# Optimization experiments

Hardware: AMD Instinct MI355X
Metric: run time of the kernel (lower is better)

Reference implementation:

```python
import jax, jax.numpy as jnp
import numpy as np

# Chambolle-Pock / Condat over-relaxed primal-dual constants (from _TVDenoiser.__init__)
TAU = 0.01
RHO = 1.99
SIGMA = 1.0 / TAU / 8.0  # 1/tau/8, 8 = Lipschitz const of D^T D in 2D
THS = 0.1                # lambda (denoise threshold)
NITER = 40
CRIT = 1e-5


def nabla2(x):
    """Forward finite differences: x (..., H, W) -> u (..., H, W, 2).
    Channel 0: diff along H (rows), channel 1: diff along W (cols); last
    row/col of each channel is zero (as in the deepinv original)."""
    dh = jnp.zeros_like(x).at[..., :-1, :].set(x[..., 1:, :] - x[..., :-1, :])
    dw = jnp.zeros_like(x).at[..., :, :-1].set(x[..., :, 1:] - x[..., :, :-1])
    return jnp.stack([dh, dw], axis=-1)


def nabla2_adjoint(u):
    """Adjoint of nabla2: u (..., H, W, 2) -> (..., H, W)."""
    v0 = u[..., :-1, :, 0]  # (..., H-1, W)
    v1 = u[..., :, :-1, 1]  # (..., H, W-1)
    out = jnp.zeros(u.shape[:-1], u.dtype)
    out = out.at[..., :-1, :].add(-v0).at[..., 1:, :].add(v0)
    out = out.at[..., :, :-1].add(-v1).at[..., :, 1:].add(v1)
    return out


def _step(x2, u2, y):
    # prox_tau_fx: (x + tau*y)/(1+tau)
    x = (x2 - TAU * nabla2_adjoint(u2) + TAU * y) / (1.0 + TAU)
    # prox_sigma_g_conj: project gradient field onto L2 ball of radius lambda
    v = u2 + SIGMA * nabla2(2.0 * x - x2)
    mag = jnp.sqrt(jnp.sum(v * v, axis=-1))  # (..., H, W)
    u = v / jnp.maximum(mag / THS, 1.0)[..., None]
    # over-relaxation
    x2n = x2 + RHO * (x - x2)
    u2n = u2 + RHO * (u - u2)
    return x2n, u2n


def setup_inputs() -> dict:
    key = jax.random.key(0)
    y = jax.random.normal(key, (8, 512, 512), dtype=jnp.float32)
    return {"y": y}


def reference(y):
    # warm restart init: x2 = y, u2 = 0 (restart branch of forward)
    u0 = jnp.zeros(y.shape + (2,), y.dtype)

    def cond(state):
        x2, u2, it, rel = state
        # original breaks at end of iteration _ if _ > 1 and rel_err < crit
        return (it < NITER) & jnp.logical_not((it >= 3) & (rel < CRIT))

    def body(state):
        x2, u2, it, _ = state
        x2n, u2n = _step(x2, u2, y)
        rel = jnp.linalg.norm((x2 - x2n).ravel()) / jnp.linalg.norm(
            x2n.ravel() + 1e-12
        )
        return (x2n, u2n, it + 1, rel)

    x2, u2, it, rel = jax.lax.while_loop(
        cond, body, (y, u0, jnp.int32(0), jnp.float32(jnp.inf))
    )
    return x2
```

## Files before the change

kernel.cpp:

```cpp
#include <hip/hip_runtime.h>


#define Hh 512
#define Ww 512
#define Bb 8
#define TS 48
#define KF 8
#define S  64
#define NT 512
#define RS 8

__global__ __launch_bounds__(NT, 3)
void tv_packed(const float*  __restrict__ y_in,
               const float4* __restrict__ st_in,
               float4* __restrict__ st_out,
               float*  __restrict__ x2_out,
               int first, int last)
{
    constexpr float TAU = 0.01f;
    constexpr float RHO = 1.99f;
    constexpr float HRHO = 0.995f;
    constexpr float SIGMA = 12.5f;
    constexpr float THS = 0.1f;
    constexpr float INV_1PT = 1.0f / 1.01f;

    __shared__ float u0B [9 * S];
    __shared__ float wTop[9 * S];

    const int b   = blockIdx.z;
    const int r0  = blockIdx.y * TS;
    const int c0  = blockIdx.x * TS;
    const int tid = threadIdx.x;
    const size_t plane = (size_t)b * (Hh * Ww);

    const int s   = tid >> 6;
    const int lc  = tid & 63;
    const int gc  = c0 - KF + lc;
    const bool colin = (gc >= 0) & (gc < Ww);
    const float sewf = (gc < Ww - 1) ? SIGMA : 0.f;
    const int lr0 = RS * s;
    const int gr0 = r0 - KF + lr0;
    const float sigBot = (gr0 + RS - 1 == Hh - 1) ? 0.f : SIGMA;

    if (tid < S) { u0B[tid] = 0.f; wTop[8 * S + tid] = 0.f; }

    float u0[RS], u1[RS], x2[RS], yv[RS], w[RS];
    unsigned tmp0 = 0u, tmp1 = 0u;

    #pragma unroll
    for (int i = 0; i < RS; ++i) {
        const int gr = gr0 + i;
        const int lr = lr0 + i;
        const bool img = colin & (gr >= 0) & (gr < Hh);
        const size_t gi = img ? (plane + (size_t)gr * Ww + gc) : plane;
        if (first) {
            float c = y_in[gi];
            c = img ? c : 0.f;
            x2[i] = c; yv[i] = c; u0[i] = 0.f; u1[i] = 0.f;
        } else {
            float4 st = st_in[gi];
            x2[i] = img ? st.x : 0.f;
            u0[i] = img ? st.y : 0.f;
            u1[i] = img ? st.z : 0.f;
            yv[i] = img ? st.w : 0.f;
        }
        unsigned tm = img ? (unsigned)min(min(lr, S - 1 - lr), min(lc, S - 1 - lc)) : 0u;
        if (i < 4) tmp0 |= tm << (8 * i);
        else       tmp1 |= tm << (8 * (i - 4));
    }
    u0B[(s + 1) * S + lc] = u0[RS - 1];
    __syncthreads();

    for (int t = 0; t < KF; ++t) {
        {
            float u0a = u0B[s * S + lc];
            #pragma unroll
            for (int i = 0; i < RS; ++i) {
                float ul = __shfl_up(u1[i], 1, 64);
                float ua = (i == 0) ? u0a : u0[i - 1];
                float adj = ua - u0[i] + ul - u1[i];
                float xv = fmaf(TAU, yv[i] - adj, x2[i]);
                w[i] = fmaf(2.0f * INV_1PT, xv, -x2[i]);
            }
            wTop[s * S + lc] = w[0];
        }
        __syncthreads();
        {
            float wbot = wTop[(s + 1) * S + lc];
            #pragma unroll
            for (int i = 0; i < RS; ++i) {
                float wr = __shfl_down(w[i], 1, 64);
                float wb = (i == RS - 1) ? wbot : w[i + 1];
                const float sig_h = (i == RS - 1) ? sigBot : SIGMA;
                float v0 = fmaf(sig_h, wb - w[i], u0[i]);
                float v1 = fmaf(sewf,  wr - w[i], u1[i]);
                float iv = fminf(THS * __builtin_amdgcn_rsqf(fmaf(v0, v0, v1 * v1)), 1.f);
                unsigned tmb = ((i < 4 ? tmp0 : tmp1) >> (8 * (i & 3))) & 255u;
                bool act = (unsigned)t < tmb;
                float r1 = act ? RHO  : 0.f;
                float rh = act ? HRHO : 0.f;
                u0[i] = fmaf(r1, fmaf(v0, iv, -u0[i]), u0[i]);
                u1[i] = fmaf(r1, fmaf(v1, iv, -u1[i]), u1[i]);
                x2[i] = fmaf(rh, w[i] - x2[i], x2[i]);
            }
            u0B[(s + 1) * S + lc] = u0[RS - 1];
        }
        __syncthreads();
    }

    if (s >= 1 && s <= 6 && lc >= KF && lc < KF + TS && gc < Ww) {
        #pragma unroll
        for (int i = 0; i < RS; ++i) {
            const int gr = gr0 + i;
            if (gr < Hh) {
                const size_t gi = plane + (size_t)gr * Ww + gc;
                if (last) x2_out[gi] = x2[i];
                else      st_out[gi] = make_float4(x2[i], u0[i], u1[i], yv[i]);
            }
        }
    }
}

__global__ __launch_bounds__(NT, 3)
void tv_sep(const float*  __restrict__ x2_in,
            const float2* __restrict__ u_in,
            const float*  __restrict__ y_in,
            float*  __restrict__ x2_out,
            float2* __restrict__ u_out,
            int first, int last)
{
    constexpr float TAU = 0.01f;
    constexpr float RHO = 1.99f;
    constexpr float HRHO = 0.995f;
    constexpr float SIGMA = 12.5f;
    constexpr float THS = 0.1f;
    constexpr float INV_1PT = 1.0f / 1.01f;

    __shared__ float u0B [9 * S];
    __shared__ float wTop[9 * S];

    const int b   = blockIdx.z;
    const int r0  = blockIdx.y * TS;
    const int c0  = blockIdx.x * TS;
    const int tid = threadIdx.x;
    const size_t plane = (size_t)b * (Hh * Ww);

    const int s   = tid >> 6;
    const int lc  = tid & 63;
    const int gc  = c0 - KF + lc;
    const bool colin = (gc >= 0) & (gc < Ww);
    const float sewf = (gc < Ww - 1) ? SIGMA : 0.f;
    const int lr0 = RS * s;
    const int gr0 = r0 - KF + lr0;
    const float sigBot = (gr0 + RS - 1 == Hh - 1) ? 0.f : SIGMA;

    if (tid < S) { u0B[tid] = 0.f; wTop[8 * S + tid] = 0.f; }

    float u0[RS], u1[RS], x2[RS], yv[RS], w[RS];
    unsigned tmp0 = 0u, tmp1 = 0u;

    #pragma unroll
    for (int i = 0; i < RS; ++i) {
        const int gr = gr0 + i;
        const int lr = lr0 + i;
        const bool img = colin & (gr >= 0) & (gr < Hh);
        float a = 0.f, c = 0.f, z0 = 0.f, z1 = 0.f;
        if (img) {
            size_t gi = plane + (size_t)gr * Ww + gc;
            c = y_in[gi];
            if (first) a = c;
            else {
                a = x2_in[gi];
                float2 uu = u_in[gi];
                z0 = uu.x; z1 = uu.y;
            }
        }
        u0[i] = z0; u1[i] = z1; x2[i] = a; yv[i] = c;
        unsigned tm = img ? (unsigned)min(min(lr, S - 1 - lr), min(lc, S - 1 - lc)) : 0u;
        if (i < 4) tmp0 |= tm << (8 * i);
        else       tmp1 |= tm << (8 * (i - 4));
    }
    u0B[(s + 1) * S + lc] = u0[RS - 1];
    __syncthreads();

    for (int t = 0; t < KF; ++t) {
        {
            float u0a = u0B[s * S + lc];
            #pragma unroll
            for (int i = 0; i < RS; ++i) {
                float ul = __shfl_up(u1[i], 1, 64);
                float ua = (i == 0) ? u0a : u0[i - 1];
                float adj = ua - u0[i] + ul - u1[i];
                float xv = fmaf(TAU, yv[i] - adj, x2[i]);
                w[i] = fmaf(2.0f * INV_1PT, xv, -x2[i]);
            }
            wTop[s * S + lc] = w[0];
        }
        __syncthreads();
        {
            float wbot = wTop[(s + 1) * S + lc];
            #pragma unroll
            for (int i = 0; i < RS; ++i) {
                float wr = __shfl_down(w[i], 1, 64);
                float wb = (i == RS - 1) ? wbot : w[i + 1];
                const float sig_h = (i == RS - 1) ? sigBot : SIGMA;
                float v0 = fmaf(sig_h, wb - w[i], u0[i]);
                float v1 = fmaf(sewf,  wr - w[i], u1[i]);
                float iv = fminf(THS * __builtin_amdgcn_rsqf(fmaf(v0, v0, v1 * v1)), 1.f);
                unsigned tmb = ((i < 4 ? tmp0 : tmp1) >> (8 * (i & 3))) & 255u;
                bool act = (unsigned)t < tmb;
                float r1 = act ? RHO  : 0.f;
                float rh = act ? HRHO : 0.f;
                u0[i] = fmaf(r1, fmaf(v0, iv, -u0[i]), u0[i]);
                u1[i] = fmaf(r1, fmaf(v1, iv, -u1[i]), u1[i]);
                x2[i] = fmaf(rh, w[i] - x2[i], x2[i]);
            }
            u0B[(s + 1) * S + lc] = u0[RS - 1];
        }
        __syncthreads();
    }

    if (s >= 1 && s <= 6 && lc >= KF && lc < KF + TS && gc < Ww) {
        #pragma unroll
        for (int i = 0; i < RS; ++i) {
            const int gr = gr0 + i;
            if (gr < Hh) {
                size_t gi = plane + (size_t)gr * Ww + gc;
                x2_out[gi] = x2[i];
                if (!last) u_out[gi] = make_float2(u0[i], u1[i]);
            }
        }
    }
}

extern "C" void kernel_launch(void* const* d_in, const int* in_sizes, int n_in,
                              void* d_out, int out_size, void* d_ws, size_t ws_size,
                              hipStream_t stream)
{
    const float* y = (const float*)d_in[0];
    float* out = (float*)d_out;
    const size_t NP = (size_t)Bb * Hh * Ww;

    dim3 grid((Ww + TS - 1) / TS, (Hh + TS - 1) / TS, Bb);

    if (ws_size >= 2 * NP * sizeof(float4)) {
        float4* stA = (float4*)d_ws;
        float4* stB = stA + NP;
        tv_packed<<<grid, NT, 0, stream>>>(y, stB, stA, out, 1, 0);
        tv_packed<<<grid, NT, 0, stream>>>(y, stA, stB, out, 0, 0);
        tv_packed<<<grid, NT, 0, stream>>>(y, stB, stA, out, 0, 0);
        tv_packed<<<grid, NT, 0, stream>>>(y, stA, stB, out, 0, 0);
        tv_packed<<<grid, NT, 0, stream>>>(y, stB, stA, out, 0, 1);
    } else {
        float*  ws  = (float*)d_ws;
        float*  x2A = ws;
        float*  x2B = ws + NP;
        float2* uA  = (float2*)(ws + 2 * NP);
        float2* uB  = (float2*)(ws + 4 * NP);
        tv_sep<<<grid, NT, 0, stream>>>(y,   uB, y, x2A, uA, 1, 0);
        tv_sep<<<grid, NT, 0, stream>>>(x2A, uA, y, x2B, uB, 0, 0);
        tv_sep<<<grid, NT, 0, stream>>>(x2B, uB, y, x2A, uA, 0, 0);
        tv_sep<<<grid, NT, 0, stream>>>(x2A, uA, y, x2B, uB, 0, 0);
        tv_sep<<<grid, NT, 0, stream>>>(x2B, uB, y, out, uA, 0, 1);
    }
}
```

Before: 223.2 us.

## Widen packed-state tiles to two columns per thread to cut halo overhead

Each thread in the packed kernel now processes two adjacent columns, widening the block tile to 128 columns with a 112-column interior. This reduces the fraction of redundant halo computation in the temporally blocked stencil. The cost is double the per-thread registers, launch bounds lowered to two blocks per SM, and fewer blocks in the grid, with a partially filled last column tile.

```diff
diff --git a/kernel.cpp b/kernel.cpp
--- a/kernel.cpp
+++ b/kernel.cpp
@@ -4,13 +4,15 @@
 #define Hh 512
 #define Ww 512
 #define Bb 8
-#define TS 48
+#define TSC 112
+#define TSR 48
 #define KF 8
-#define S  64
+#define SC 128
+#define SR 64
 #define NT 512
 #define RS 8
 
-__global__ __launch_bounds__(NT, 3)
+__global__ __launch_bounds__(NT, 2)
 void tv_packed(const float*  __restrict__ y_in,
                const float4* __restrict__ st_in,
                float4* __restrict__ st_out,
@@ -24,6 +26,156 @@
     constexpr float THS = 0.1f;
     constexpr float INV_1PT = 1.0f / 1.01f;
 
+    __shared__ float u0B [9 * SC];
+    __shared__ float wTop[9 * SC];
+
+    const int b   = blockIdx.z;
+    const int r0  = blockIdx.y * TSR;
+    const int c0  = blockIdx.x * TSC;
+    const int tid = threadIdx.x;
+    const size_t plane = (size_t)b * (Hh * Ww);
+
+    const int s     = tid >> 6;
+    const int lc    = tid & 63;
+    const int lcol0 = 2 * lc;
+    const int gc0   = c0 - KF + lcol0;
+    const bool colin0 = (gc0 >= 0) & (gc0 < Ww);
+    const bool colin1 = (gc0 + 1 >= 0) & (gc0 + 1 < Ww);
+    const float sewf0 = (gc0     < Ww - 1) ? SIGMA : 0.f;
+    const float sewf1 = (gc0 + 1 < Ww - 1) ? SIGMA : 0.f;
+    const int lr0 = RS * s;
+    const int gr0 = r0 - KF + lr0;
+    const float sigBot = (gr0 + RS - 1 == Hh - 1) ? 0.f : SIGMA;
+
+    if (tid < SC) { u0B[tid] = 0.f; wTop[8 * SC + tid] = 0.f; }
+
+    float x2[RS][2], u0[RS][2], u1[RS][2], yv[RS][2], w[RS][2];
+    unsigned tmp[4] = {0u, 0u, 0u, 0u};
+
+    #pragma unroll
+    for (int i = 0; i < RS; ++i) {
+        const int gr = gr0 + i;
+        const int lr = lr0 + i;
+        const bool rin = (gr >= 0) & (gr < Hh);
+        #pragma unroll
+        for (int c = 0; c < 2; ++c) {
+            const bool img = rin & (c ? colin1 : colin0);
+            const size_t gi = img ? (plane + (size_t)gr * Ww + (gc0 + c)) : plane;
+            if (first) {
+                float cy = y_in[gi]; cy = img ? cy : 0.f;
+                x2[i][c] = cy; yv[i][c] = cy; u0[i][c] = 0.f; u1[i][c] = 0.f;
+            } else {
+                float4 st = st_in[gi];
+                x2[i][c] = img ? st.x : 0.f;
+                u0[i][c] = img ? st.y : 0.f;
+                u1[i][c] = img ? st.z : 0.f;
+                yv[i][c] = img ? st.w : 0.f;
+            }
+            const int lcol = lcol0 + c;
+            unsigned tm = img ? (unsigned)min(min(lr, SR - 1 - lr),
+                                              min(lcol, SC - 1 - lcol)) : 0u;
+            const int k = 2 * i + c;
+            tmp[k >> 2] |= tm << (8 * (k & 3));
+        }
+    }
+    *(float2*)&u0B[(s + 1) * SC + lcol0] = make_float2(u0[RS - 1][0], u0[RS - 1][1]);
+    __syncthreads();
+
+    for (int t = 0; t < KF; ++t) {
+        {
+            float2 ua2 = *(float2*)&u0B[s * SC + lcol0];
+            #pragma unroll
+            for (int i = 0; i < RS; ++i) {
+                float ul0 = __shfl_up(u1[i][1], 1, 64);
+                float ul1 = u1[i][0];
+                float ua_0 = (i == 0) ? ua2.x : u0[i - 1][0];
+                float ua_1 = (i == 0) ? ua2.y : u0[i - 1][1];
+                float adj0 = ua_0 - u0[i][0] + ul0 - u1[i][0];
+                float adj1 = ua_1 - u0[i][1] + ul1 - u1[i][1];
+                float xv0 = fmaf(TAU, yv[i][0] - adj0, x2[i][0]);
+                float xv1 = fmaf(TAU, yv[i][1] - adj1, x2[i][1]);
+                w[i][0] = fmaf(2.0f * INV_1PT, xv0, -x2[i][0]);
+                w[i][1] = fmaf(2.0f * INV_1PT, xv1, -x2[i][1]);
+            }
+            *(float2*)&wTop[s * SC + lcol0] = make_float2(w[0][0], w[0][1]);
+        }
+        __syncthreads();
+        {
+            float2 wb2 = *(float2*)&wTop[(s + 1) * SC + lcol0];
+            #pragma unroll
+            for (int i = 0; i < RS; ++i) {
+                float wr1 = __shfl_down(w[i][0], 1, 64);
+                float wr0 = w[i][1];
+                float wb_0 = (i == RS - 1) ? wb2.x : w[i + 1][0];
+                float wb_1 = (i == RS - 1) ? wb2.y : w[i + 1][1];
+                const float sig_h = (i == RS - 1) ? sigBot : SIGMA;
+
+                float v00 = fmaf(sig_h, wb_0 - w[i][0], u0[i][0]);
+                float v10 = fmaf(sewf0, wr0 - w[i][0], u1[i][0]);
+                float iv0 = fminf(THS * __builtin_amdgcn_rsqf(fmaf(v00, v00, v10 * v10)), 1.f);
+                float v01 = fmaf(sig_h, wb_1 - w[i][1], u0[i][1]);
+                float v11 = fmaf(sewf1, wr1 - w[i][1], u1[i][1]);
+                float iv1 = fminf(THS * __builtin_amdgcn_rsqf(fmaf(v01, v01, v11 * v11)), 1.f);
+
+                const int k0 = 2 * i, k1 = 2 * i + 1;
+                unsigned tm0 = (tmp[k0 >> 2] >> (8 * (k0 & 3))) & 255u;
+                unsigned tm1 = (tmp[k1 >> 2] >> (8 * (k1 & 3))) & 255u;
+                bool a0 = (unsigned)t < tm0;
+                bool a1 = (unsigned)t < tm1;
+                float r10 = a0 ? RHO : 0.f, rh0 = a0 ? HRHO : 0.f;
+                float r11 = a1 ? RHO : 0.f, rh1 = a1 ? HRHO : 0.f;
+
+                u0[i][0] = fmaf(r10, fmaf(v00, iv0, -u0[i][0]), u0[i][0]);
+                u1[i][0] = fmaf(r10, fmaf(v10, iv0, -u1[i][0]), u1[i][0]);
+                x2[i][0] = fmaf(rh0, w[i][0] - x2[i][0], x2[i][0]);
+                u0[i][1] = fmaf(r11, fmaf(v01, iv1, -u0[i][1]), u0[i][1]);
+                u1[i][1] = fmaf(r11, fmaf(v11, iv1, -u1[i][1]), u1[i][1]);
+                x2[i][1] = fmaf(rh1, w[i][1] - x2[i][1], x2[i][1]);
+            }
+            *(float2*)&u0B[(s + 1) * SC + lcol0] = make_float2(u0[RS - 1][0], u0[RS - 1][1]);
+        }
+        __syncthreads();
+    }
+
+    if (s >= 1 && s <= 6) {
+        #pragma unroll
+        for (int c = 0; c < 2; ++c) {
+            const int lcol = lcol0 + c;
+            const int gc   = gc0 + c;
+            if (lcol >= KF && lcol < KF + TSC && gc < Ww) {
+                #pragma unroll
+                for (int i = 0; i < RS; ++i) {
+                    const int gr = gr0 + i;
+                    if (gr < Hh) {
+                        const size_t gi = plane + (size_t)gr * Ww + gc;
+                        if (last) x2_out[gi] = x2[i][c];
+                        else      st_out[gi] = make_float4(x2[i][c], u0[i][c],
+                                                           u1[i][c], yv[i][c]);
+                    }
+                }
+            }
+        }
+    }
+}
+
+#define TS 48
+#define S  64
+
+__global__ __launch_bounds__(NT, 3)
+void tv_sep(const float*  __restrict__ x2_in,
+            const float2* __restrict__ u_in,
+            const float*  __restrict__ y_in,
+            float*  __restrict__ x2_out,
+            float2* __restrict__ u_out,
+            int first, int last)
+{
+    constexpr float TAU = 0.01f;
+    constexpr float RHO = 1.99f;
+    constexpr float HRHO = 0.995f;
+    constexpr float SIGMA = 12.5f;
+    constexpr float THS = 0.1f;
+    constexpr float INV_1PT = 1.0f / 1.01f;
+
     __shared__ float u0B [9 * S];
     __shared__ float wTop[9 * S];
 
@@ -52,18 +204,18 @@
         const int gr = gr0 + i;
         const int lr = lr0 + i;
         const bool img = colin & (gr >= 0) & (gr < Hh);
-        const size_t gi = img ? (plane + (size_t)gr * Ww + gc) : plane;
-        if (first) {
-            float c = y_in[gi];
-            c = img ? c : 0.f;
-            x2[i] = c; yv[i] = c; u0[i] = 0.f; u1[i] = 0.f;
-        } else {
-            float4 st = st_in[gi];
-            x2[i] = img ? st.x : 0.f;
-            u0[i] = img ? st.y : 0.f;
-            u1[i] = img ? st.z : 0.f;
-            yv[i] = img ? st.w : 0.f;
-        }
+        float a = 0.f, c = 0.f, z0 = 0.f, z1 = 0.f;
+        if (img) {
+            size_t gi = plane + (size_t)gr * Ww + gc;
+            c = y_in[gi];
+            if (first) a = c;
+            else {
+                a = x2_in[gi];
+                float2 uu = u_in[gi];
+                z0 = uu.x; z1 = uu.y;
+            }
+        }
+        u0[i] = z0; u1[i] = z1; x2[i] = a; yv[i] = c;
         unsigned tm = img ? (unsigned)min(min(lr, S - 1 - lr), min(lc, S - 1 - lc)) : 0u;
         if (i < 4) tmp0 |= tm << (8 * i);
         else       tmp1 |= tm << (8 * (i - 4));
@@ -113,118 +265,6 @@
         for (int i = 0; i < RS; ++i) {
             const int gr = gr0 + i;
             if (gr < Hh) {
-                const size_t gi = plane + (size_t)gr * Ww + gc;
-                if (last) x2_out[gi] = x2[i];
-                else      st_out[gi] = make_float4(x2[i], u0[i], u1[i], yv[i]);
-            }
-        }
-    }
-}
-
-__global__ __launch_bounds__(NT, 3)
-void tv_sep(const float*  __restrict__ x2_in,
-            const float2* __restrict__ u_in,
-            const float*  __restrict__ y_in,
-            float*  __restrict__ x2_out,
-            float2* __restrict__ u_out,
-            int first, int last)
-{
-    constexpr float TAU = 0.01f;
-    constexpr float RHO = 1.99f;
-    constexpr float HRHO = 0.995f;
-    constexpr float SIGMA = 12.5f;
-    constexpr float THS = 0.1f;
-    constexpr float INV_1PT = 1.0f / 1.01f;
-
-    __shared__ float u0B [9 * S];
-    __shared__ float wTop[9 * S];
-
-    const int b   = blockIdx.z;
-    const int r0  = blockIdx.y * TS;
-    const int c0  = blockIdx.x * TS;
-    const int tid = threadIdx.x;
-    const size_t plane = (size_t)b * (Hh * Ww);
-
-    const int s   = tid >> 6;
-    const int lc  = tid & 63;
-    const int gc  = c0 - KF + lc;
-    const bool colin = (gc >= 0) & (gc < Ww);
-    const float sewf = (gc < Ww - 1) ? SIGMA : 0.f;
-    const int lr0 = RS * s;
-    const int gr0 = r0 - KF + lr0;
-    const float sigBot = (gr0 + RS - 1 == Hh - 1) ? 0.f : SIGMA;
-
-    if (tid < S) { u0B[tid] = 0.f; wTop[8 * S + tid] = 0.f; }
-
-    float u0[RS], u1[RS], x2[RS], yv[RS], w[RS];
-    unsigned tmp0 = 0u, tmp1 = 0u;
-
-    #pragma unroll
-    for (int i = 0; i < RS; ++i) {
-        const int gr = gr0 + i;
-        const int lr = lr0 + i;
-        const bool img = colin & (gr >= 0) & (gr < Hh);
-        float a = 0.f, c = 0.f, z0 = 0.f, z1 = 0.f;
-        if (img) {
-            size_t gi = plane + (size_t)gr * Ww + gc;
-            c = y_in[gi];
-            if (first) a = c;
-            else {
-                a = x2_in[gi];
-                float2 uu = u_in[gi];
-                z0 = uu.x; z1 = uu.y;
-            }
-        }
-        u0[i] = z0; u1[i] = z1; x2[i] = a; yv[i] = c;
-        unsigned tm = img ? (unsigned)min(min(lr, S - 1 - lr), min(lc, S - 1 - lc)) : 0u;
-        if (i < 4) tmp0 |= tm << (8 * i);
-        else       tmp1 |= tm << (8 * (i - 4));
-    }
-    u0B[(s + 1) * S + lc] = u0[RS - 1];
-    __syncthreads();
-
-    for (int t = 0; t < KF; ++t) {
-        {
-            float u0a = u0B[s * S + lc];
-            #pragma unroll
-            for (int i = 0; i < RS; ++i) {
-                float ul = __shfl_up(u1[i], 1, 64);
-                float ua = (i == 0) ? u0a : u0[i - 1];
-                float adj = ua - u0[i] + ul - u1[i];
-                float xv = fmaf(TAU, yv[i] - adj, x2[i]);
-                w[i] = fmaf(2.0f * INV_1PT, xv, -x2[i]);
-            }
-            wTop[s * S + lc] = w[0];
-        }
-        __syncthreads();
-        {
-            float wbot = wTop[(s + 1) * S + lc];
-            #pragma unroll
-            for (int i = 0; i < RS; ++i) {
-                float wr = __shfl_down(w[i], 1, 64);
-                float wb = (i == RS - 1) ? wbot : w[i + 1];
-                const float sig_h = (i == RS - 1) ? sigBot : SIGMA;
-                float v0 = fmaf(sig_h, wb - w[i], u0[i]);
-                float v1 = fmaf(sewf,  wr - w[i], u1[i]);
-                float iv = fminf(THS * __builtin_amdgcn_rsqf(fmaf(v0, v0, v1 * v1)), 1.f);
-                unsigned tmb = ((i < 4 ? tmp0 : tmp1) >> (8 * (i & 3))) & 255u;
-                bool act = (unsigned)t < tmb;
-                float r1 = act ? RHO  : 0.f;
-                float rh = act ? HRHO : 0.f;
-                u0[i] = fmaf(r1, fmaf(v0, iv, -u0[i]), u0[i]);
-                u1[i] = fmaf(r1, fmaf(v1, iv, -u1[i]), u1[i]);
-                x2[i] = fmaf(rh, w[i] - x2[i], x2[i]);
-            }
-            u0B[(s + 1) * S + lc] = u0[RS - 1];
-        }
-        __syncthreads();
-    }
-
-    if (s >= 1 && s <= 6 && lc >= KF && lc < KF + TS && gc < Ww) {
-        #pragma unroll
-        for (int i = 0; i < RS; ++i) {
-            const int gr = gr0 + i;
-            if (gr < Hh) {
                 size_t gi = plane + (size_t)gr * Ww + gc;
                 x2_out[gi] = x2[i];
                 if (!last) u_out[gi] = make_float2(u0[i], u1[i]);
@@ -241,11 +281,10 @@
     float* out = (float*)d_out;
     const size_t NP = (size_t)Bb * Hh * Ww;
 
-    dim3 grid((Ww + TS - 1) / TS, (Hh + TS - 1) / TS, Bb);
-
     if (ws_size >= 2 * NP * sizeof(float4)) {
         float4* stA = (float4*)d_ws;
         float4* stB = stA + NP;
+        dim3 grid((Ww + TSC - 1) / TSC, (Hh + TSR - 1) / TSR, Bb);
         tv_packed<<<grid, NT, 0, stream>>>(y, stB, stA, out, 1, 0);
         tv_packed<<<grid, NT, 0, stream>>>(y, stA, stB, out, 0, 0);
         tv_packed<<<grid, NT, 0, stream>>>(y, stB, stA, out, 0, 0);
@@ -257,6 +296,7 @@
         float*  x2B = ws + NP;
         float2* uA  = (float2*)(ws + 2 * NP);
         float2* uB  = (float2*)(ws + 4 * NP);
+        dim3 grid((Ww + TS - 1) / TS, (Hh + TS - 1) / TS, Bb);
         tv_sep<<<grid, NT, 0, stream>>>(y,   uB, y, x2A, uA, 1, 0);
         tv_sep<<<grid, NT, 0, stream>>>(x2A, uA, y, x2B, uB, 0, 0);
         tv_sep<<<grid, NT, 0, stream>>>(x2B, uB, y, x2A, uA, 0, 0);
```

New measurement: 222.6 us. About the same (-0.3%).
